# Performance work log

Hardware: AMD Instinct MI355X
Metric: run time of the kernel (lower is better)

Reference implementation:

```python
import jax, jax.numpy as jnp
import numpy as np

N_STATE = 32  # SSM states per channel (S4D)


def lrelu(x):
    return jnp.where(x >= 0, x, 0.3 * x)


def conv1d(x, w, b, stride=1, pad=0, dil=1):
    # x: [B,C,L], w: [O,I,K]
    y = jax.lax.conv_general_dilated(
        x, w, (stride,), [(pad, pad)], rhs_dilation=(dil,),
        dimension_numbers=('NCH', 'OIH', 'NCH'))
    return y + b[None, :, None]


def batchnorm(x, g, b, eps=1e-5):
    # training-mode BatchNorm1d: stats over (B, L) per channel
    m = jnp.mean(x, axis=(0, 2), keepdims=True)
    v = jnp.var(x, axis=(0, 2), keepdims=True)
    return (x - m) * jax.lax.rsqrt(v + eps) * g[None, :, None] + b[None, :, None]


def s4_layer(u, log_dt, C2, D):
    # Diagonal S4 (S4D-Lin): u [B,H,L] -> y [B,H,L]; causal FFT conv + skip
    H, N = C2.shape[0], C2.shape[1]
    L = u.shape[-1]
    A = -0.5 + 1j * jnp.pi * jnp.arange(N, dtype=jnp.float32)            # [N]
    dtA = jnp.exp(log_dt)[:, None] * A[None, :]                          # [H,N]
    C = (C2[..., 0] + 1j * C2[..., 1]) * (jnp.exp(dtA) - 1.0) / A        # [H,N]
    vand = jnp.exp(dtA[:, :, None] * jnp.arange(L, dtype=jnp.float32))   # [H,N,L]
    K = 2.0 * jnp.real(jnp.einsum('hn,hnl->hl', C, vand))                # [H,L]
    uf = jnp.fft.rfft(u, n=2 * L)
    Kf = jnp.fft.rfft(K, n=2 * L)
    y = jnp.fft.irfft(uf * Kf[None], n=2 * L)[..., :L]
    return y + D[None, :, None] * u


def down_block(x, s4p, convs, g, b):
    # dilated residual inception down block: S4 then 4 stride-4 dilated convs
    x = s4_layer(x, *s4p)
    d1 = batchnorm(conv1d(x, convs[0][0], convs[0][1], 4, 1, 1), g, b)
    d2 = batchnorm(lrelu(conv1d(x, convs[1][0], convs[1][1], 4, 2, 2)), g, b)
    d3 = batchnorm(lrelu(conv1d(x, convs[2][0], convs[2][1], 4, 4, 4)), g, b)
    d4 = batchnorm(lrelu(conv1d(x, convs[3][0], convs[3][1], 4, 8, 8)), g, b)
    return jnp.concatenate([d1, d2, d3, d4], axis=1)


def setup_inputs() -> dict:
    key = jax.random.key(0)
    ks = iter(jax.random.split(key, 64))

    def nrm(shape, scale=1.0):
        return jax.random.normal(next(ks), shape, jnp.float32) * scale

    def logdt(H):
        lo, hi = np.log(0.001), np.log(0.1)
        return jax.random.uniform(next(ks), (H,), jnp.float32) * (hi - lo) + lo

    B, L, DIN = 16, 8192, 2
    inp = {}
    inp['x'] = nrm((B, L, DIN))
    inp['enc_w'] = nrm((64, DIN, 1), (1.0 / DIN) ** 0.5)
    inp['enc_b'] = jnp.zeros((64,), jnp.float32)
    for pfx, H in (('s4a', 64), ('s4b', 256), ('s4c', 1024)):
        inp[pfx + '_log_dt'] = logdt(H)
        inp[pfx + '_C'] = nrm((H, N_STATE, 2), 0.5 ** 0.5)
        inp[pfx + '_D'] = nrm((H,))
    for blk, C in (('b1', 64), ('b2', 256)):
        sc = (1.0 / (C * 3)) ** 0.5
        for i in range(1, 5):
            inp[f'{blk}_w{i}'] = nrm((C, C, 3), sc)
            inp[f'{blk}_b{i}'] = nrm((C,), 0.02)
    inp['bn1_g'] = jnp.ones((64,), jnp.float32)
    inp['bn1_b'] = jnp.zeros((64,), jnp.float32)
    inp['bn2_g'] = jnp.ones((256,), jnp.float32)
    inp['bn2_b'] = jnp.zeros((256,), jnp.float32)
    inp['dec1_w'] = nrm((256, 1024, 1), (1.0 / 1024) ** 0.5)
    inp['dec1_b'] = jnp.zeros((256,), jnp.float32)
    inp['dec2_w'] = nrm((1, 256, 1), (1.0 / 256) ** 0.5)
    inp['dec2_b'] = jnp.zeros((1,), jnp.float32)
    return inp


def reference(x, enc_w, enc_b,
              s4a_log_dt, s4a_C, s4a_D,
              b1_w1, b1_b1, b1_w2, b1_b2, b1_w3, b1_b3, b1_w4, b1_b4, bn1_g, bn1_b,
              s4b_log_dt, s4b_C, s4b_D,
              b2_w1, b2_b1, b2_w2, b2_b2, b2_w3, b2_b3, b2_w4, b2_b4, bn2_g, bn2_b,
              s4c_log_dt, s4c_C, s4c_D,
              dec1_w, dec1_b, dec2_w, dec2_b):
    h = conv1d(jnp.transpose(x, (0, 2, 1)), enc_w, enc_b)                 # [B,64,L]
    x1 = down_block(h, (s4a_log_dt, s4a_C, s4a_D),
                    [(b1_w1, b1_b1), (b1_w2, b1_b2), (b1_w3, b1_b3), (b1_w4, b1_b4)],
                    bn1_g, bn1_b)                                          # [B,256,L/4]
    x2 = down_block(x1, (s4b_log_dt, s4b_C, s4b_D),
                    [(b2_w1, b2_b1), (b2_w2, b2_b2), (b2_w3, b2_b3), (b2_w4, b2_b4)],
                    bn2_g, bn2_b)                                          # [B,1024,L/16]
    x3 = s4_layer(x2, s4c_log_dt, s4c_C, s4c_D)
    y = conv1d(conv1d(x3, dec1_w, dec1_b), dec2_w, dec2_b)                 # [B,1,L/16]
    ff = jnp.squeeze(y, axis=1)                                            # [B,L/16]
    return ff[..., -1:]                                                    # [B,1]
```

## Files before the change

kernel.cpp:

```cpp
#include <hip/hip_runtime.h>
#include <math.h>

#define PI_F 3.14159265358979323846f

typedef __attribute__((ext_vector_type(8))) short short8;
typedef __attribute__((ext_vector_type(4))) float f32x4;

__device__ __forceinline__ unsigned short f2bf(float f) {
    unsigned int u = __float_as_uint(f);
    unsigned int r = (u + 0x7fffu + ((u >> 16) & 1u)) >> 16;
    return (unsigned short)r;
}
__device__ __forceinline__ float bf2f(unsigned short v) {
    return __uint_as_float((unsigned int)v << 16);
}

__global__ __launch_bounds__(256) void prep_w(
    const float* __restrict__ w0, const float* __restrict__ w1,
    const float* __restrict__ w2, const float* __restrict__ w3,
    const float* __restrict__ w4, const float* __restrict__ w5,
    const float* __restrict__ w6, const float* __restrict__ w7,
    unsigned short* __restrict__ wprep)
{
    int id = blockIdx.y;
    const float* src; int Cin; size_t doff;
    switch (id) {
        case 0: src = w0; Cin = 64;  doff = 0;      break;
        case 1: src = w1; Cin = 64;  doff = 12288;  break;
        case 2: src = w2; Cin = 64;  doff = 24576;  break;
        case 3: src = w3; Cin = 64;  doff = 36864;  break;
        case 4: src = w4; Cin = 256; doff = 49152;  break;
        case 5: src = w5; Cin = 256; doff = 245760; break;
        case 6: src = w6; Cin = 256; doff = 442368; break;
        default: src = w7; Cin = 256; doff = 638976; break;
    }
    int e = blockIdx.x * 256 + threadIdx.x;
    if (e >= Cin * Cin * 3) return;
    int kb  = e / (Cin * 32);
    int rem = e - kb * (Cin * 32);
    int o   = rem >> 5;
    int kk  = rem & 31;
    int cch = kb / 6, t6 = kb % 6, k = t6 >> 1, chalf = t6 & 1;
    int c = cch * 64 + chalf * 32 + kk;
    wprep[doff + e] = f2bf(src[((size_t)o * Cin + c) * 3 + k]);
}

__global__ __launch_bounds__(128) void prep_s4_both(
    const float* __restrict__ ldt_a, const float* __restrict__ C2_a,
    const float* __restrict__ Dv_a,
    unsigned short* __restrict__ TA_a, unsigned short* __restrict__ VA_a,
    float* __restrict__ rs_a, float* __restrict__ Vrs_a,
    const float* __restrict__ ldt_b, const float* __restrict__ C2_b,
    const float* __restrict__ Dv_b,
    unsigned short* __restrict__ TA_b, unsigned short* __restrict__ VA_b,
    float* __restrict__ rs_b, float* __restrict__ Vrs_b)
{
    int bid = blockIdx.x, t = threadIdx.x;
    const float* log_dt; const float* C2; const float* Dv;
    unsigned short* TA; unsigned short* VA; float* rs; float* Vrs; int h;
    if (bid < 64) { h = bid;      log_dt = ldt_a; C2 = C2_a; Dv = Dv_a; TA = TA_a; VA = VA_a; rs = rs_a; Vrs = Vrs_a; }
    else          { h = bid - 64; log_dt = ldt_b; C2 = C2_b; Dv = Dv_b; TA = TA_b; VA = VA_b; rs = rs_b; Vrs = Vrs_b; }
    __shared__ float cn[64];
    __shared__ float sK[128];
    __shared__ unsigned short s_w[128 * 66];
    float dt = expf(log_dt[h]);
    if (t < 32) {
        int n = t;
        float e = expf(-0.5f*dt);
        float s_, c_; sincosf(PI_F*dt*n, &s_, &c_);
        float wr = e*c_, wi = e*s_;
        float ar = -0.5f, ai = PI_F*n;
        float den = 1.f/(ar*ar + ai*ai);
        float tr = wr - 1.f, ti = wi;
        float qr = (tr*ar + ti*ai)*den;
        float qi = (ti*ar - tr*ai)*den;
        float c2r = C2[((size_t)h*32+n)*2], c2i = C2[((size_t)h*32+n)*2+1];
        cn[2*n]   = 2.f*(c2r*qr - c2i*qi);
        cn[2*n+1] = 2.f*(c2r*qi + c2i*qr);
        float e128 = expf(-64.f*dt);
        float s2, c2v; sincosf(PI_F*dt*n*128.f, &s2, &c2v);
        float pr = 1.f - e128*c2v, pim = -e128*s2;
        float dr = 1.f - wr, di = -wi;
        float dd = 1.f/(dr*dr + di*di);
        Vrs[(size_t)h*64 + 2*n]   = (pr*dr + pim*di)*dd;
        Vrs[(size_t)h*64 + 2*n+1] = (pim*dr - pr*di)*dd;
    }
    __syncthreads();
    {
        float em = expf(-0.5f*dt*t);
        float Kt = 0.f;
        for (int n = 0; n < 32; n++) {
            float s_, c_; sincosf(PI_F*dt*(float)(n*t), &s_, &c_);
            Kt += cn[2*n]*em*c_ - cn[2*n+1]*em*s_;
        }
        sK[t] = Kt + (t == 0 ? Dv[h] : 0.f);
    }
    if (t < 64) {
        int n = t >> 1, ri = t & 1;
        float e = expf(-0.5f*dt);
        float s_, c_; sincosf(PI_F*dt*n, &s_, &c_);
        float wr = e*c_, wi = e*s_;
        float crn = cn[2*n], cin = cn[2*n+1];
        float pr = wr, pim = wi;
        for (int m = 0; m < 128; m++) {
            float re = crn*pr - cin*pim;
            float im = crn*pim + cin*pr;
            s_w[m*66 + t] = f2bf(ri ? -im : re);
            float nr = pr*wr - pim*wi;
            float ni = pr*wi + pim*wr;
            pr = nr; pim = ni;
        }
    } else {
        int r = t - 64; int n = r >> 1, ri = r & 1;
        float e = expf(-0.5f*dt);
        float s_, c_; sincosf(PI_F*dt*n, &s_, &c_);
        float wr = e*c_, wi = e*s_;
        float cr2 = 1.f, ci2 = 0.f;
        for (int kb = 3; kb >= 0; kb--) {
            unsigned short buf[32];
            for (int kk = 31; kk >= 0; kk--) {
                buf[kk] = f2bf(ri ? ci2 : cr2);
                float nr = cr2*wr - ci2*wi;
                float ni = cr2*wi + ci2*wr;
                cr2 = nr; ci2 = ni;
            }
            uint4* dst = (uint4*)&VA[(((size_t)h*4 + kb)*64 + r)*32];
            uint4* src = (uint4*)buf;
            dst[0]=src[0]; dst[1]=src[1]; dst[2]=src[2]; dst[3]=src[3];
        }
    }
    __syncthreads();
    {
        float acc = 0.f;
        for (int tau = 0; tau <= t; tau++) acc += sK[tau];
        rs[(size_t)h*128 + t] = acc;
    }
    for (int kb = 0; kb < 4; kb++) {
        unsigned short tb[32];
#pragma unroll
        for (int kk = 0; kk < 32; kk++) {
            int col = kb*32 + kk;
            tb[kk] = f2bf((col <= t) ? sK[t - col] : 0.f);
        }
        uint4* dst = (uint4*)&TA[(((size_t)h*6 + kb)*128 + t)*32];
        uint4* src = (uint4*)tb;
        dst[0]=src[0]; dst[1]=src[1]; dst[2]=src[2]; dst[3]=src[3];
    }
    for (int i = t; i < 1024; i += 128) {
        int kb = i >> 9;
        int rem = i & 511;
        int m = rem >> 2, kkg = rem & 3;
        *(uint4*)&TA[(((size_t)h*6 + 4 + kb)*128 + m)*32 + kkg*8] =
            *(const uint4*)&s_w[m*66 + kb*32 + kkg*8];
    }
}

template<int NCH, int LOGNCH, bool ENC>
__global__ __launch_bounds__(256) void s4_layer_fused(
    const unsigned short* __restrict__ u, const float* __restrict__ xg,
    const float* __restrict__ ew, const float* __restrict__ ebv,
    const unsigned short* __restrict__ VA,
    const float* __restrict__ Vrs, const unsigned short* __restrict__ TA,
    const float* __restrict__ rs, const float* __restrict__ sc,
    const float* __restrict__ sh, const float* __restrict__ log_dt,
    unsigned short* __restrict__ yout)
{
    const int L = NCH * 128;
    __shared__ unsigned short s_u[64*200];
    __shared__ unsigned short s_s[64*72];
    __shared__ float sE[64*68];
    int h = blockIdx.y;
    int tid = threadIdx.x;
    int lane = tid & 63, wid = tid >> 6;
    int nl = lane & 15, g = lane >> 4;
    int col0 = blockIdx.x * 64;
    float scv = sc ? sc[h] : 1.f;
    float shv = sh ? sh[h] : 0.f;

    if constexpr (ENC) {
        float w0e = ew[2*h], w1e = ew[2*h+1], bbe = ebv[h];
        for (int i = tid; i < 1024; i += 256) {
            int cl = i >> 4, o = i & 15;
            int col = col0 + cl; int b = col >> LOGNCH, c = col & (NCH - 1);
            const float* xp = xg + ((size_t)b*8192 + (size_t)(c*128 + o*8))*2;
            float4 a0 = *(const float4*)xp;
            float4 a1 = *(const float4*)(xp + 4);
            float4 a2 = *(const float4*)(xp + 8);
            float4 a3 = *(const float4*)(xp + 12);
            ushort4 q0, q1;
            q0.x = f2bf(fmaf(w0e, a0.x, fmaf(w1e, a0.y, bbe)));
            q0.y = f2bf(fmaf(w0e, a0.z, fmaf(w1e, a0.w, bbe)));
            q0.z = f2bf(fmaf(w0e, a1.x, fmaf(w1e, a1.y, bbe)));
            q0.w = f2bf(fmaf(w0e, a1.z, fmaf(w1e, a1.w, bbe)));
            q1.x = f2bf(fmaf(w0e, a2.x, fmaf(w1e, a2.y, bbe)));
            q1.y = f2bf(fmaf(w0e, a2.z, fmaf(w1e, a2.w, bbe)));
            q1.z = f2bf(fmaf(w0e, a3.x, fmaf(w1e, a3.y, bbe)));
            q1.w = f2bf(fmaf(w0e, a3.z, fmaf(w1e, a3.w, bbe)));
            *(ushort4*)&s_u[cl*200 + o*8]     = q0;
            *(ushort4*)&s_u[cl*200 + o*8 + 4] = q1;
        }
    } else {
        for (int i = tid; i < 1024; i += 256) {
            int cl = i >> 4, o = i & 15;
            int col = col0 + cl; int b = col >> LOGNCH, c = col & (NCH - 1);
            *(uint4*)&s_u[cl*200 + o*8] =
                *(const uint4*)&u[((size_t)h*16 + b)*L + c*128 + o*8];
        }
    }
    __syncthreads();

    {
        int cl = wid*16 + nl;
        f32x4 acc[4];
#pragma unroll
        for (int mt = 0; mt < 4; mt++) acc[mt] = (f32x4){0.f,0.f,0.f,0.f};
#pragma unroll
        for (int kb = 0; kb < 4; kb++) {
            short8 bf = *(const short8*)&s_u[cl*200 + kb*32 + g*8];
#pragma unroll
            for (int mt = 0; mt < 4; mt++) {
                short8 af = *(const short8*)(VA + (((size_t)h*4 + kb)*64 + mt*16 + nl)*32 + g*8);
                acc[mt] = __builtin_amdgcn_mfma_f32_16x16x32_bf16(af, bf, acc[mt], 0, 0, 0);
            }
        }
#pragma unroll
        for (int mt = 0; mt < 4; mt++) {
            int j0 = mt*16 + g*4;
            float4 vr = *(const float4*)(Vrs + (size_t)h*64 + j0);
            sE[cl*68 + j0 + 0] = fmaf(scv, acc[mt][0], shv*vr.x);
            sE[cl*68 + j0 + 1] = fmaf(scv, acc[mt][1], shv*vr.y);
            sE[cl*68 + j0 + 2] = fmaf(scv, acc[mt][2], shv*vr.z);
            sE[cl*68 + j0 + 3] = fmaf(scv, acc[mt][3], shv*vr.w);
        }
    }
    __syncthreads();

    constexpr int NB = 64 / NCH;
    if (tid < NB * 32) {
        int bl = tid >> 5, n = tid & 31;
        float dt = expf(log_dt[h]);
        float e = expf(-0.5f * dt);
        float s_, c_; sincosf(PI_F * dt * n, &s_, &c_);
        float Wr = e*c_, Wi = e*s_;
#pragma unroll
        for (int i = 0; i < 7; i++) { float r = Wr*Wr - Wi*Wi; float im = 2.f*Wr*Wi; Wr = r; Wi = im; }
        float Sr = 0.f, Si = 0.f;
        for (int c2 = 0; c2 < NCH; c2++) {
            float* ep = &sE[(bl*NCH + c2)*68 + 2*n];
            float er = ep[0], ei = ep[1];
            ep[0] = Sr; ep[1] = Si;
            float r  = fmaf(Wr, Sr, fmaf(-Wi, Si, er));
            float im = fmaf(Wi, Sr, fmaf( Wr, Si, ei));
            Sr = r; Si = im;
        }
    }
    __syncthreads();

    for (int i = tid*4; i < 4096; i += 1024) {
        int cl = i >> 6, j = i & 63;
        ushort4 q;
        q.x = f2bf(sE[cl*68 + j]);
        q.y = f2bf(sE[cl*68 + j+1]);
        q.z = f2bf(sE[cl*68 + j+2]);
        q.w = f2bf(sE[cl*68 + j+3]);
        *(ushort4*)&s_s[cl*72 + j] = q;
    }
    __syncthreads();

    f32x4 accT[2][4], accW[2][4];
#pragma unroll
    for (int a = 0; a < 2; a++)
#pragma unroll
        for (int j = 0; j < 4; j++) { accT[a][j] = (f32x4){0,0,0,0}; accW[a][j] = (f32x4){0,0,0,0}; }
#pragma unroll
    for (int kb = 0; kb < 4; kb++) {
        short8 bfr[4];
#pragma unroll
        for (int j = 0; j < 4; j++)
            bfr[j] = *(const short8*)&s_u[(j*16 + nl)*200 + kb*32 + g*8];
#pragma unroll
        for (int mt2 = 0; mt2 < 2; mt2++) {
            int mtile = wid*2 + mt2;
            short8 af = *(const short8*)&TA[(((size_t)h*6 + kb)*128 + mtile*16 + nl)*32 + g*8];
#pragma unroll
            for (int j = 0; j < 4; j++)
                accT[mt2][j] = __builtin_amdgcn_mfma_f32_16x16x32_bf16(af, bfr[j], accT[mt2][j], 0, 0, 0);
        }
    }
#pragma unroll
    for (int kw = 0; kw < 2; kw++) {
        short8 bfr[4];
#pragma unroll
        for (int j = 0; j < 4; j++)
            bfr[j] = *(const short8*)&s_s[(j*16 + nl)*72 + kw*32 + g*8];
#pragma unroll
        for (int mt2 = 0; mt2 < 2; mt2++) {
            int mtile = wid*2 + mt2;
            short8 af = *(const short8*)&TA[(((size_t)h*6 + 4 + kw)*128 + mtile*16 + nl)*32 + g*8];
#pragma unroll
            for (int j = 0; j < 4; j++)
                accW[mt2][j] = __builtin_amdgcn_mfma_f32_16x16x32_bf16(af, bfr[j], accW[mt2][j], 0, 0, 0);
        }
    }
#pragma unroll
    for (int mt2 = 0; mt2 < 2; mt2++) {
        int m0 = (wid*2 + mt2)*16 + g*4;
        float4 rsv = *(const float4*)&rs[(size_t)h*128 + m0];
#pragma unroll
        for (int j = 0; j < 4; j++) {
            int col = col0 + j*16 + nl; int b = col >> LOGNCH, c = col & (NCH - 1);
            ushort4 q;
            q.x = f2bf(fmaf(scv, accT[mt2][j][0], shv*rsv.x) + accW[mt2][j][0]);
            q.y = f2bf(fmaf(scv, accT[mt2][j][1], shv*rsv.y) + accW[mt2][j][1]);
            q.z = f2bf(fmaf(scv, accT[mt2][j][2], shv*rsv.z) + accW[mt2][j][2]);
            q.w = f2bf(fmaf(scv, accT[mt2][j][3], shv*rsv.w) + accW[mt2][j][3]);
            *(ushort4*)&yout[((size_t)h*16 + b)*L + c*128 + m0] = q;
        }
    }
}

template<int CIN, int TBLK>
__global__ __launch_bounds__(256, 2) void conv_mfma4(
    const unsigned short* __restrict__ u, const unsigned short* __restrict__ wp,
    const float* __restrict__ bs0, const float* __restrict__ bs1,
    const float* __restrict__ bs2, const float* __restrict__ bs3,
    unsigned short* __restrict__ out, int Lin, int Lout)
{
    constexpr int F     = TBLK / 16;
    constexpr int NPOS  = TBLK * 4 + 16;
    constexpr int Q     = NPOS / 4;
    constexpr int NITEM = (NPOS / 8) * 64;
    constexpr int NLD   = (NITEM + 255) / 256;
    constexpr int NCC   = CIN / 64;
    constexpr int NBUF  = (NCC > 1) ? 2 : 1;
    constexpr int BUFSZ = 4 * Q * 64;
    __shared__ unsigned short s_in[NBUF * BUFSZ];

    int tid = threadIdx.x;
    int lane = tid & 63, wid = tid >> 6;
    int nl = lane & 15, g = lane >> 4;
    int t0 = blockIdx.x * TBLK;
    int b  = blockIdx.y;
    int og = blockIdx.z * 64;
    const int P0 = t0 * 4 - 8;
    const int DIL = 1 << wid;

    f32x4 acc[4][F];
#pragma unroll
    for (int m = 0; m < 4; m++)
#pragma unroll
        for (int f = 0; f < F; f++) acc[m][f] = (f32x4){0.f,0.f,0.f,0.f};

    uint4 stg[NLD];

    auto stage_load = [&](int ccbase) {
#pragma unroll
        for (int j = 0; j < NLD; j++) {
            int i = tid + 256 * j;
            uint4 v; v.x = 0u; v.y = 0u; v.z = 0u; v.w = 0u;
            if (i < NITEM) {
                int ch = i & 63, po = i >> 6;
                int p = P0 + po * 8;
                const unsigned short* gp = u + ((size_t)(ccbase + ch)*16 + b)*Lin;
                if (p >= 0 && p + 8 <= Lin) {
                    v = *(const uint4*)(gp + p);
                } else {
                    alignas(16) unsigned short t8[8];
#pragma unroll
                    for (int j2 = 0; j2 < 8; j2++) {
                        int pj = p + j2;
                        t8[j2] = ((unsigned)pj < (unsigned)Lin) ? gp[pj] : (unsigned short)0;
                    }
                    v = *(const uint4*)t8;
                }
            }
            stg[j] = v;
        }
    };
    auto stage_write = [&](int bufidx) {
        unsigned short* sb = s_in + bufidx * BUFSZ;
#pragma unroll
        for (int j = 0; j < NLD; j++) {
            int i = tid + 256 * j;
            if (i < NITEM) {
                int ch = i & 63, po = i >> 6;
                alignas(16) unsigned short t8[8];
                *(uint4*)t8 = stg[j];
#pragma unroll
                for (int jj = 0; jj < 8; jj++) {
                    int pl = po * 8 + jj;
                    int row = (pl & 3) * Q + (pl >> 2);
                    sb[row * 64 + (ch ^ ((row & 7) << 3))] = t8[jj];
                }
            }
        }
    };

    stage_load(0);
    stage_write(0);
    __syncthreads();

#pragma unroll
    for (int cc = 0; cc < NCC; cc++) {
        if (cc + 1 < NCC) stage_load((cc + 1) * 64);
        const unsigned short* sb = s_in + (NBUF > 1 ? (cc & 1) * BUFSZ : 0);
#pragma unroll
        for (int k = 0; k < 3; ++k) {
            const int off = (k - 1) * DIL + 8;
            const int r = off & 3, s = off >> 2;
#pragma unroll
            for (int chalf = 0; chalf < 2; ++chalf) {
                int kb = cc * 6 + k * 2 + chalf;
                short8 bfr[F];
#pragma unroll
                for (int f = 0; f < F; ++f) {
                    int q = f*16 + nl + s;
                    int row = r * Q + q;
                    bfr[f] = *(const short8*)&sb[row * 64 +
                        ((((chalf << 2) | g) ^ (row & 7)) << 3)];
                }
#pragma unroll
                for (int m = 0; m < 4; ++m) {
                    short8 afrag = *(const short8*)&wp[(size_t)wid*(3*CIN*CIN) +
                        ((size_t)kb*CIN + og + m*16 + nl)*32 + g*8];
#pragma unroll
                    for (int f = 0; f < F; ++f)
                        acc[m][f] = __builtin_amdgcn_mfma_f32_16x16x32_bf16(afrag, bfr[f], acc[m][f], 0, 0, 0);
                }
            }
        }
        if (cc + 1 < NCC) {
            __syncthreads();
            stage_write((cc + 1) & 1);
            __syncthreads();
        }
    }

    const float* bp = (wid == 0) ? bs0 : (wid == 1) ? bs1 : (wid == 2) ? bs2 : bs3;
#pragma unroll
    for (int m = 0; m < 4; ++m) {
#pragma unroll
        for (int f = 0; f < F; ++f) {
            int t = t0 + f*16 + nl;
#pragma unroll
            for (int r2 = 0; r2 < 4; ++r2) {
                int o = og + m*16 + g*4 + r2;
                float v = acc[m][f][r2] + bp[o];
                if (wid) v = v >= 0.f ? v : 0.3f*v;
                out[((size_t)(wid*CIN + o)*16 + b)*Lout + t] = f2bf(v);
            }
        }
    }
}

__global__ __launch_bounds__(256) void bn_stats(
    const unsigned short* __restrict__ x, const float* __restrict__ g,
    const float* __restrict__ bb, float* __restrict__ sc, float* __restrict__ sh,
    int n, int gmask)
{
    int ch = blockIdx.x;
    const unsigned short* xp = x + (size_t)ch * n;
    float s1 = 0.f, s2 = 0.f;
    for (int i = threadIdx.x*8; i < n; i += 2048) {
        uint4 raw = *(const uint4*)(xp + i);
        unsigned short us[8]; *(uint4*)us = raw;
#pragma unroll
        for (int j = 0; j < 8; j++) {
            float v = bf2f(us[j]);
            s1 += v; s2 += v*v;
        }
    }
    for (int o = 32; o > 0; o >>= 1) { s1 += __shfl_down(s1, o); s2 += __shfl_down(s2, o); }
    __shared__ float p1[4], p2[4];
    int wid = threadIdx.x >> 6;
    if ((threadIdx.x & 63) == 0) { p1[wid] = s1; p2[wid] = s2; }
    __syncthreads();
    if (threadIdx.x == 0) {
        s1 = p1[0] + p1[1] + p1[2] + p1[3];
        s2 = p2[0] + p2[1] + p2[2] + p2[3];
        float m = s1 / n;
        float var = s2 / n - m*m;
        float rstd = rsqrtf(var + 1e-5f);
        float scale = g[ch & gmask] * rstd;
        sc[ch] = scale;
        sh[ch] = fmaf(-m, scale, bb[ch & gmask]);
    }
}

__global__ __launch_bounds__(256) void s4c_all(
    const unsigned short* __restrict__ u,
    const float* __restrict__ sc, const float* __restrict__ sh,
    const float* __restrict__ log_dt, const float* __restrict__ C2,
    const float* __restrict__ Dv, float* __restrict__ x3last)
{
    __shared__ float sE[64 * 68];
    __shared__ float red[16 * 33];
    __shared__ unsigned short sVA[4 * 64 * 32];
    __shared__ alignas(16) float sVrs[64];
    int h = blockIdx.x;
    int tid = threadIdx.x;
    int lane = tid & 63, wid = tid >> 6;
    int nl = lane & 15, g = lane >> 4;
    float scv = sc[h], shv = sh[h];
    float dt = expf(log_dt[h]);

    {
        int t = lane, n = t >> 1, ri = t & 1;
        int kb = wid;
        float e = expf(-0.5f*dt);
        float s_, c_; sincosf(PI_F*dt*n, &s_, &c_);
        float wr = e*c_, wi = e*s_;
        int e0 = 96 - kb*32;
        float em0 = expf(-0.5f*dt*(float)e0);
        float s0, c0; sincosf(PI_F*dt*(float)n*(float)e0, &s0, &c0);
        float cr2 = em0*c0, ci2 = em0*s0;
        alignas(16) unsigned short buf[32];
        for (int kk = 31; kk >= 0; kk--) {
            buf[kk] = f2bf(ri ? ci2 : cr2);
            float nr = cr2*wr - ci2*wi;
            float ni = cr2*wi + ci2*wr;
            cr2 = nr; ci2 = ni;
        }
        int key = (t >> 1) & 3;
        uint4* dst = (uint4*)&sVA[(kb*64 + t)*32];
        uint4* src4 = (uint4*)buf;
#pragma unroll
        for (int cc = 0; cc < 4; cc++) dst[cc ^ key] = src4[cc];
        if (wid == 0 && ri == 0) {
            float e128 = expf(-64.f*dt);
            float s2, c2v; sincosf(PI_F*dt*n*128.f, &s2, &c2v);
            float pr = 1.f - e128*c2v, pim = -e128*s2;
            float dr = 1.f - wr, di = -wi;
            float dd = 1.f/(dr*dr + di*di);
            sVrs[2*n]   = (pr*dr + pim*di)*dd;
            sVrs[2*n+1] = (pim*dr - pr*di)*dd;
        }
    }
    __syncthreads();

    int rkey = (nl >> 1) & 3;
    {
        int col = wid*16 + nl;
        int b = col >> 2, c = col & 3;
        const unsigned short* up = u + ((size_t)h*16 + b)*512 + c*128;
        f32x4 acc[4];
#pragma unroll
        for (int mt = 0; mt < 4; mt++) acc[mt] = (f32x4){0.f,0.f,0.f,0.f};
#pragma unroll
        for (int kb = 0; kb < 4; kb++) {
            short8 bf = *(const short8*)(up + kb*32 + g*8);
#pragma unroll
            for (int mt = 0; mt < 4; mt++) {
                short8 af = *(const short8*)&sVA[(kb*64 + mt*16 + nl)*32 + ((g ^ rkey) << 3)];
                acc[mt] = __builtin_amdgcn_mfma_f32_16x16x32_bf16(af, bf, acc[mt], 0, 0, 0);
            }
        }
#pragma unroll
        for (int mt = 0; mt < 4; mt++) {
            int j0 = mt*16 + g*4;
            float4 vr = *(const float4*)&sVrs[j0];
            sE[col*68 + j0 + 0] = fmaf(scv, acc[mt][0], shv*vr.x);
            sE[col*68 + j0 + 1] = fmaf(scv, acc[mt][1], shv*vr.y);
            sE[col*68 + j0 + 2] = fmaf(scv, acc[mt][2], shv*vr.z);
            sE[col*68 + j0 + 3] = fmaf(scv, acc[mt][3], shv*vr.w);
        }
    }
    __syncthreads();

    if (tid < 64) {
        int n = lane >> 1, bh = lane & 1;
        float e = expf(-0.5f * dt);
        float s_, c_; sincosf(PI_F * dt * n, &s_, &c_);
        float wr = e*c_, wi = e*s_;
        float ar = -0.5f, ai = PI_F * n;
        float den = 1.f / (ar*ar + ai*ai);
        float tr = wr - 1.f, ti = wi;
        float qr = (tr*ar + ti*ai) * den;
        float qi = (ti*ar - tr*ai) * den;
        float c2r = C2[((size_t)h*32 + n)*2], c2i = C2[((size_t)h*32 + n)*2 + 1];
        float crv = c2r*qr - c2i*qi, civ = c2r*qi + c2i*qr;
        float Wr = wr, Wi = wi;
#pragma unroll
        for (int i = 0; i < 7; i++) { float r = Wr*Wr - Wi*Wi; float im = 2.f*Wr*Wi; Wr = r; Wi = im; }
#pragma unroll
        for (int b2 = 0; b2 < 8; b2++) {
            int b = bh*8 + b2;
            float Sr = 0.f, Si = 0.f;
#pragma unroll
            for (int c = 0; c < 4; c++) {
                int col = b*4 + c;
                float er = sE[col*68 + 2*n], ei = sE[col*68 + 2*n + 1];
                float r  = fmaf(Wr, Sr, fmaf(-Wi, Si, er));
                float im = fmaf(Wi, Sr, fmaf( Wr, Si, ei));
                Sr = r; Si = im;
            }
            red[b*33 + n] = crv*Sr - civ*Si;
        }
    }
    __syncthreads();
    if (tid < 16) {
        int b = tid;
        float s = 0.f;
        for (int n2 = 0; n2 < 32; n2++) s += red[b*33 + n2];
        float uv = fmaf(scv, bf2f(u[((size_t)h*16 + b)*512 + 511]), shv);
        x3last[b*1024 + h] = 2.f*s + Dv[h]*uv;
    }
}

__global__ __launch_bounds__(256) void dec_kernel(
    const float* __restrict__ x3last, const float* __restrict__ w1, const float* __restrict__ b1,
    const float* __restrict__ w2, const float* __restrict__ b2, float* __restrict__ out)
{
    __shared__ float xs[1024];
    int b = blockIdx.x, tid = threadIdx.x;
    for (int i = tid; i < 1024; i += 256) xs[i] = x3last[b*1024 + i];
    __syncthreads();
    float z = b1[tid];
    const float* wpt = w1 + (size_t)tid*1024;
    for (int i = 0; i < 1024; i += 4) {
        float4 wv = *(const float4*)(wpt + i);
        z = fmaf(wv.x, xs[i],   z);
        z = fmaf(wv.y, xs[i+1], z);
        z = fmaf(wv.z, xs[i+2], z);
        z = fmaf(wv.w, xs[i+3], z);
    }
    float v = w2[tid] * z;
    for (int o = 32; o > 0; o >>= 1) v += __shfl_down(v, o);
    __shared__ float ps[4];
    if ((tid & 63) == 0) ps[tid >> 6] = v;
    __syncthreads();
    if (tid == 0) out[b] = ps[0] + ps[1] + ps[2] + ps[3] + b2[0];
}

extern "C" void kernel_launch(void* const* d_in, const int* in_sizes, int n_in,
                              void* d_out, int out_size, void* d_ws, size_t ws_size,
                              hipStream_t stream)
{
    const float* x       = (const float*)d_in[0];
    const float* enc_w   = (const float*)d_in[1];
    const float* enc_b   = (const float*)d_in[2];
    const float* s4a_ldt = (const float*)d_in[3];
    const float* s4a_C   = (const float*)d_in[4];
    const float* s4a_D   = (const float*)d_in[5];
    const float* s4b_ldt = (const float*)d_in[6];
    const float* s4b_C   = (const float*)d_in[7];
    const float* s4b_D   = (const float*)d_in[8];
    const float* s4c_ldt = (const float*)d_in[9];
    const float* s4c_C   = (const float*)d_in[10];
    const float* s4c_D   = (const float*)d_in[11];
    const float* b1w[4] = {(const float*)d_in[12], (const float*)d_in[14], (const float*)d_in[16], (const float*)d_in[18]};
    const float* b1b[4] = {(const float*)d_in[13], (const float*)d_in[15], (const float*)d_in[17], (const float*)d_in[19]};
    const float* b2w[4] = {(const float*)d_in[20], (const float*)d_in[22], (const float*)d_in[24], (const float*)d_in[26]};
    const float* b2b[4] = {(const float*)d_in[21], (const float*)d_in[23], (const float*)d_in[25], (const float*)d_in[27]};
    const float* bn1_g  = (const float*)d_in[28];
    const float* bn1_b  = (const float*)d_in[29];
    const float* bn2_g  = (const float*)d_in[30];
    const float* bn2_b  = (const float*)d_in[31];
    const float* dec1_w = (const float*)d_in[32];
    const float* dec1_b = (const float*)d_in[33];
    const float* dec2_w = (const float*)d_in[34];
    const float* dec2_b = (const float*)d_in[35];
    float* out = (float*)d_out;

    char* ws = (char*)d_ws;
    unsigned short* u3    = (unsigned short*)(ws);
    unsigned short* ya    = (unsigned short*)(ws + 16777216);
    unsigned short* yb    = ya;
    unsigned short* u2    = (unsigned short*)(ws + 33554432);
    unsigned short* wprep = (unsigned short*)(ws + 88080384);
    unsigned short* TA_a  = (unsigned short*)(ws + 89751552);
    unsigned short* TA_b  = (unsigned short*)(ws + 92897280);
    unsigned short* VA_a  = (unsigned short*)(ws + 105480192);
    unsigned short* VA_b  = (unsigned short*)(ws + 106528768);
    float*          rs_a  = (float*)(ws + 110723072);
    float*          rs_b  = (float*)(ws + 110755840);
    float*          Vrs_a = (float*)(ws + 110886912);
    float*          Vrs_b = (float*)(ws + 110903296);
    float*          smallp= (float*)(ws + 110968832);
    float* sc1 = smallp;
    float* sh1 = smallp + 256;
    float* sc2 = smallp + 512;
    float* sh2 = smallp + 1536;
    float* x3l = smallp + 2560;

    prep_w<<<dim3(768, 8), 256, 0, stream>>>(b1w[0], b1w[1], b1w[2], b1w[3],
                                             b2w[0], b2w[1], b2w[2], b2w[3], wprep);
    prep_s4_both<<<320, 128, 0, stream>>>(
        s4a_ldt, s4a_C, s4a_D, TA_a, VA_a, rs_a, Vrs_a,
        s4b_ldt, s4b_C, s4b_D, TA_b, VA_b, rs_b, Vrs_b);

    s4_layer_fused<64,6,true><<<dim3(16, 64), 256, 0, stream>>>(
        nullptr, x, enc_w, enc_b, VA_a, Vrs_a, TA_a, rs_a, nullptr, nullptr, s4a_ldt, ya);

    conv_mfma4<64,32><<<dim3(64, 16, 1), 256, 0, stream>>>(
        ya, wprep, b1b[0], b1b[1], b1b[2], b1b[3], u2, 8192, 2048);
    bn_stats<<<256, 256, 0, stream>>>(u2, bn1_g, bn1_b, sc1, sh1, 16*2048, 63);

    s4_layer_fused<16,4,false><<<dim3(4, 256), 256, 0, stream>>>(
        u2, nullptr, nullptr, nullptr, VA_b, Vrs_b, TA_b, rs_b, sc1, sh1, s4b_ldt, yb);

    conv_mfma4<256,64><<<dim3(8, 16, 4), 256, 0, stream>>>(
        yb, wprep + 49152, b2b[0], b2b[1], b2b[2], b2b[3], u3, 2048, 512);
    bn_stats<<<1024, 256, 0, stream>>>(u3, bn2_g, bn2_b, sc2, sh2, 16*512, 255);

    s4c_all<<<1024, 256, 0, stream>>>(u3, sc2, sh2, s4c_ldt, s4c_C, s4c_D, x3l);

    dec_kernel<<<16, 256, 0, stream>>>(x3l, dec1_w, dec1_b, dec2_w, dec2_b, out);
}
```

Measured before the change: 302.4 us.

## Merge weight and S4 prep kernels, single-buffer conv LDS, enlarge first conv tile

Folds the bf16 weight-repacking kernel into the S4 parameter prep kernel so a single launch does both. Extra blocks beyond the first 320 each handle 256 weight elements. The dilated conv kernel drops its double-buffered shared memory and uses one buffer, which is safe because writes already sit between barriers; this halves LDS use and may raise occupancy for the 256-channel conv. The first conv now uses a 64-wide time tile with half the blocks, trading grid parallelism for more reuse of each weight fragment.

```diff
diff --git a/kernel.cpp b/kernel.cpp
--- a/kernel.cpp
+++ b/kernel.cpp
@@ -15,37 +15,7 @@
     return __uint_as_float((unsigned int)v << 16);
 }
 
-__global__ __launch_bounds__(256) void prep_w(
-    const float* __restrict__ w0, const float* __restrict__ w1,
-    const float* __restrict__ w2, const float* __restrict__ w3,
-    const float* __restrict__ w4, const float* __restrict__ w5,
-    const float* __restrict__ w6, const float* __restrict__ w7,
-    unsigned short* __restrict__ wprep)
-{
-    int id = blockIdx.y;
-    const float* src; int Cin; size_t doff;
-    switch (id) {
-        case 0: src = w0; Cin = 64;  doff = 0;      break;
-        case 1: src = w1; Cin = 64;  doff = 12288;  break;
-        case 2: src = w2; Cin = 64;  doff = 24576;  break;
-        case 3: src = w3; Cin = 64;  doff = 36864;  break;
-        case 4: src = w4; Cin = 256; doff = 49152;  break;
-        case 5: src = w5; Cin = 256; doff = 245760; break;
-        case 6: src = w6; Cin = 256; doff = 442368; break;
-        default: src = w7; Cin = 256; doff = 638976; break;
-    }
-    int e = blockIdx.x * 256 + threadIdx.x;
-    if (e >= Cin * Cin * 3) return;
-    int kb  = e / (Cin * 32);
-    int rem = e - kb * (Cin * 32);
-    int o   = rem >> 5;
-    int kk  = rem & 31;
-    int cch = kb / 6, t6 = kb % 6, k = t6 >> 1, chalf = t6 & 1;
-    int c = cch * 64 + chalf * 32 + kk;
-    wprep[doff + e] = f2bf(src[((size_t)o * Cin + c) * 3 + k]);
-}
-
-__global__ __launch_bounds__(128) void prep_s4_both(
+__global__ __launch_bounds__(128) void prep_all(
     const float* __restrict__ ldt_a, const float* __restrict__ C2_a,
     const float* __restrict__ Dv_a,
     unsigned short* __restrict__ TA_a, unsigned short* __restrict__ VA_a,
@@ -53,9 +23,35 @@
     const float* __restrict__ ldt_b, const float* __restrict__ C2_b,
     const float* __restrict__ Dv_b,
     unsigned short* __restrict__ TA_b, unsigned short* __restrict__ VA_b,
-    float* __restrict__ rs_b, float* __restrict__ Vrs_b)
+    float* __restrict__ rs_b, float* __restrict__ Vrs_b,
+    const float* __restrict__ w0, const float* __restrict__ w1,
+    const float* __restrict__ w2, const float* __restrict__ w3,
+    const float* __restrict__ w4, const float* __restrict__ w5,
+    const float* __restrict__ w6, const float* __restrict__ w7,
+    unsigned short* __restrict__ wprep)
 {
     int bid = blockIdx.x, t = threadIdx.x;
+    if (bid >= 320) {
+        const float* wsrc[8] = {w0, w1, w2, w3, w4, w5, w6, w7};
+        int e0 = (bid - 320) * 256 + t;
+#pragma unroll
+        for (int half = 0; half < 2; half++) {
+            int e = e0 + half * 128;
+            if (e < 835584) {
+                int id; int doff; int Cin;
+                if (e < 49152) { id = e / 12288; doff = id * 12288; Cin = 64; }
+                else { id = 4 + (e - 49152) / 196608; doff = 49152 + (id - 4) * 196608; Cin = 256; }
+                int el = e - doff;
+                int kb = el / (Cin * 32);
+                int rem = el - kb * (Cin * 32);
+                int o = rem >> 5, kk = rem & 31;
+                int cch = kb / 6, t6 = kb % 6, k = t6 >> 1, chalf = t6 & 1;
+                int c = cch * 64 + chalf * 32 + kk;
+                wprep[e] = f2bf(wsrc[id][((size_t)o * Cin + c) * 3 + k]);
+            }
+        }
+        return;
+    }
     const float* log_dt; const float* C2; const float* Dv;
     unsigned short* TA; unsigned short* VA; float* rs; float* Vrs; int h;
     if (bid < 64) { h = bid;      log_dt = ldt_a; C2 = C2_a; Dv = Dv_a; TA = TA_a; VA = VA_a; rs = rs_a; Vrs = Vrs_a; }
@@ -332,9 +328,8 @@
     constexpr int NITEM = (NPOS / 8) * 64;
     constexpr int NLD   = (NITEM + 255) / 256;
     constexpr int NCC   = CIN / 64;
-    constexpr int NBUF  = (NCC > 1) ? 2 : 1;
     constexpr int BUFSZ = 4 * Q * 64;
-    __shared__ unsigned short s_in[NBUF * BUFSZ];
+    __shared__ unsigned short s_in[BUFSZ];
 
     int tid = threadIdx.x;
     int lane = tid & 63, wid = tid >> 6;
@@ -377,8 +372,7 @@
             stg[j] = v;
         }
     };
-    auto stage_write = [&](int bufidx) {
-        unsigned short* sb = s_in + bufidx * BUFSZ;
+    auto stage_write = [&]() {
 #pragma unroll
         for (int j = 0; j < NLD; j++) {
             int i = tid + 256 * j;
@@ -390,20 +384,19 @@
                 for (int jj = 0; jj < 8; jj++) {
                     int pl = po * 8 + jj;
                     int row = (pl & 3) * Q + (pl >> 2);
-                    sb[row * 64 + (ch ^ ((row & 7) << 3))] = t8[jj];
+                    s_in[row * 64 + (ch ^ ((row & 7) << 3))] = t8[jj];
                 }
             }
         }
     };
 
     stage_load(0);
-    stage_write(0);
+    stage_write();
     __syncthreads();
 
 #pragma unroll
     for (int cc = 0; cc < NCC; cc++) {
         if (cc + 1 < NCC) stage_load((cc + 1) * 64);
-        const unsigned short* sb = s_in + (NBUF > 1 ? (cc & 1) * BUFSZ : 0);
 #pragma unroll
         for (int k = 0; k < 3; ++k) {
             const int off = (k - 1) * DIL + 8;
@@ -416,7 +409,7 @@
                 for (int f = 0; f < F; ++f) {
                     int q = f*16 + nl + s;
                     int row = r * Q + q;
-                    bfr[f] = *(const short8*)&sb[row * 64 +
+                    bfr[f] = *(const short8*)&s_in[row * 64 +
                         ((((chalf << 2) | g) ^ (row & 7)) << 3)];
                 }
 #pragma unroll
@@ -431,7 +424,7 @@
         }
         if (cc + 1 < NCC) {
             __syncthreads();
-            stage_write((cc + 1) & 1);
+            stage_write();
             __syncthreads();
         }
     }
@@ -683,16 +676,15 @@
     float* sh2 = smallp + 1536;
     float* x3l = smallp + 2560;
 
-    prep_w<<<dim3(768, 8), 256, 0, stream>>>(b1w[0], b1w[1], b1w[2], b1w[3],
-                                             b2w[0], b2w[1], b2w[2], b2w[3], wprep);
-    prep_s4_both<<<320, 128, 0, stream>>>(
+    prep_all<<<3584, 128, 0, stream>>>(
         s4a_ldt, s4a_C, s4a_D, TA_a, VA_a, rs_a, Vrs_a,
-        s4b_ldt, s4b_C, s4b_D, TA_b, VA_b, rs_b, Vrs_b);
+        s4b_ldt, s4b_C, s4b_D, TA_b, VA_b, rs_b, Vrs_b,
+        b1w[0], b1w[1], b1w[2], b1w[3], b2w[0], b2w[1], b2w[2], b2w[3], wprep);
 
     s4_layer_fused<64,6,true><<<dim3(16, 64), 256, 0, stream>>>(
         nullptr, x, enc_w, enc_b, VA_a, Vrs_a, TA_a, rs_a, nullptr, nullptr, s4a_ldt, ya);
 
-    conv_mfma4<64,32><<<dim3(64, 16, 1), 256, 0, stream>>>(
+    conv_mfma4<64,64><<<dim3(32, 16, 1), 256, 0, stream>>>(
         ya, wprep, b1b[0], b1b[1], b1b[2], b1b[3], u2, 8192, 2048);
     bn_stats<<<256, 256, 0, stream>>>(u2, bn1_g, bn1_b, sc1, sh1, 16*2048, 63);
 
```

Result: slower. 347.6 us (+14.9%).
